# Performance work log

Hardware: AMD Instinct MI355X
Metric: run time of the kernel (lower is better)

Reference implementation:

```python
import jax, jax.numpy as jnp
import numpy as np

RATE_NUM = 8
MAX_RATE = 256
C = 256


def setup_inputs() -> dict:
    key = jax.random.key(0)
    k1, k2, k3, k4 = jax.random.split(key, 4)
    B, H, W = 4, 32, 32
    x = jax.random.normal(k1, (B, MAX_RATE, H, W), dtype=jnp.float32)
    indexes = jax.random.randint(k2, (B * H * W,), 0, RATE_NUM, dtype=jnp.int64)
    # kaiming_normal_(a=sqrt(5)) on (rate_num, max_rate, C): fan_in = C (last dim),
    # gain = sqrt(2/(1+a^2)) = sqrt(1/3), std = gain/sqrt(fan_in)
    std = np.sqrt(1.0 / 3.0) / np.sqrt(C)
    weight = jax.random.normal(k3, (RATE_NUM, MAX_RATE, C), dtype=jnp.float32) * std
    bound = 1.0 / np.sqrt(RATE_NUM)
    bias = jax.random.uniform(k4, (RATE_NUM, C), dtype=jnp.float32, minval=-bound, maxval=bound)
    return {"x": x, "indexes": indexes, "weight": weight, "bias": bias}


def reference(x, indexes, weight, bias):
    B, R, H, W = x.shape  # R == max_rate
    L = H * W
    x_blr = x.reshape(B, R, L).transpose(0, 2, 1)          # (B, L, R)
    w = weight[indexes].reshape(B, L, R, -1)               # (B, L, R, C)
    b = bias[indexes].reshape(B, L, -1)                    # (B, L, C)
    out = jnp.einsum('blr,blrc->blc', x_blr, w) + b        # per-token GEMV
    return out.reshape(B, H, W, -1).transpose(0, 3, 1, 2)  # (B, C, H, W)
```

## Files before the change

kernel.cpp:

```cpp
#include <hip/hip_runtime.h>


#define C_DIM 256
#define KD    256
#define LDP   132

typedef __attribute__((ext_vector_type(8))) short bf16x8;
typedef __attribute__((ext_vector_type(4))) float f32x4;

__device__ inline unsigned pk2(float a, float b) {
    union { float f; unsigned u; } x, y; x.f = a; y.f = b;
    return ((x.u + 0x8000u) >> 16) | ((y.u + 0x8000u) & 0xFFFF0000u);
}

__global__ __launch_bounds__(256) void prep_kernel(
    const float* __restrict__ x, const float* __restrict__ w,
    unsigned* __restrict__ wbd, unsigned* __restrict__ xbd)
{
    const int g = blockIdx.x * 256 + threadIdx.x;
    if (blockIdx.x < 256) {
        const int f  = g * 4;
        const int j  = f >> 15;
        const int ct = (f >> 14) & 1;
        const int kp = (f >> 7) & 127;
        const int cl = f & 124;
        const float4 a = *(const float4*)(w + ((j * 256 + 2 * kp    ) << 8) + ct * 128 + cl);
        const float4 b = *(const float4*)(w + ((j * 256 + 2 * kp + 1) << 8) + ct * 128 + cl);
        uint4 o;
        o.x = pk2(a.x, b.x); o.y = pk2(a.y, b.y);
        o.z = pk2(a.z, b.z); o.w = pk2(a.w, b.w);
        *(uint4*)(wbd + f) = o;
    } else {
        const int g2 = g - 65536;
        const int f  = g2 * 4;
        const int b_ = f >> 17;
        const int lt = (f >> 14) & 7;
        const int kp = (f >> 7) & 127;
        const int ll = f & 124;
        const float4 a = *(const float4*)(x + ((b_ * 256 + 2 * kp    ) << 10) + lt * 128 + ll);
        const float4 c = *(const float4*)(x + ((b_ * 256 + 2 * kp + 1) << 10) + lt * 128 + ll);
        uint4 o;
        o.x = pk2(a.x, c.x); o.y = pk2(a.y, c.y);
        o.z = pk2(a.z, c.z); o.w = pk2(a.w, c.w);
        *(uint4*)(xbd + f) = o;
    }
}

__global__ __launch_bounds__(512, 4) void fused_mfma_kernel(
    const unsigned* __restrict__ wbd,
    const unsigned* __restrict__ xbd,
    const int*      __restrict__ idx,
    const float*    __restrict__ bias,
    float*          __restrict__ out)
{
    const int t    = threadIdx.x;
    const int lane = t & 63;
    const int wav  = t >> 6;
    const int quad = lane >> 4;
    const int li   = lane & 15;

    const int j    = blockIdx.z;
    const int ct   = blockIdx.x;
    const int cb0  = ct * 128;
    const int lg0b = blockIdx.y * 128;
    const int b    = lg0b >> 10;
    const int l0b  = lg0b & 1023;
    const int lt   = (lg0b >> 7) & 7;

    __shared__ unsigned Asl[2][32 * LDP];
    __shared__ unsigned Bsl[2][32 * LDP];

    const unsigned* __restrict__ wsrc = wbd + ((j * 2 + ct) << 14);
    const unsigned* __restrict__ xsrc = xbd + ((b * 8 + lt) << 14);

    const int u0 = t, u1 = 512 + t;
    const int la0 = (u0 >> 5) * LDP + (u0 & 31) * 4;
    const int la1 = (u1 >> 5) * LDP + (u1 & 31) * 4;

    const int wc = wav & 3;
    const int wl = wav >> 2;
    const int c_locb = wc * 32;
    const int l_locb = wl * 64;

    f32x4 acc[2][4];
    #pragma unroll
    for (int mt = 0; mt < 2; ++mt)
        #pragma unroll
        for (int nt = 0; nt < 4; ++nt)
            acc[mt][nt] = (f32x4){0.f, 0.f, 0.f, 0.f};

    uint4 a0 = *(const uint4*)(wsrc + u0 * 4);
    uint4 a1 = *(const uint4*)(wsrc + u1 * 4);
    uint4 b0 = *(const uint4*)(xsrc + u0 * 4);
    uint4 b1 = *(const uint4*)(xsrc + u1 * 4);
    *(uint4*)&Asl[0][la0] = a0;
    *(uint4*)&Asl[0][la1] = a1;
    *(uint4*)&Bsl[0][la0] = b0;
    *(uint4*)&Bsl[0][la1] = b1;
    __syncthreads();

    #pragma unroll
    for (int p = 0; p < 4; ++p) {
        if (p < 3) {
            const int off = (p + 1) * 4096;
            a0 = *(const uint4*)(wsrc + off + u0 * 4);
            a1 = *(const uint4*)(wsrc + off + u1 * 4);
            b0 = *(const uint4*)(xsrc + off + u0 * 4);
            b1 = *(const uint4*)(xsrc + off + u1 * 4);
        }

        const unsigned* __restrict__ Ab = Asl[p & 1];
        const unsigned* __restrict__ Bb = Bsl[p & 1];
        #pragma unroll
        for (int h = 0; h < 2; ++h) {
            const int rbase = h * 16 + quad * 4;
            bf16x8 af[2], bfr[4];
            #pragma unroll
            for (int mt = 0; mt < 2; ++mt) {
                const int cl = c_locb + mt * 16 + li;
                uint4 u;
                u.x = Ab[(rbase + 0) * LDP + cl];
                u.y = Ab[(rbase + 1) * LDP + cl];
                u.z = Ab[(rbase + 2) * LDP + cl];
                u.w = Ab[(rbase + 3) * LDP + cl];
                af[mt] = __builtin_bit_cast(bf16x8, u);
            }
            #pragma unroll
            for (int nt = 0; nt < 4; ++nt) {
                const int ll = l_locb + nt * 16 + li;
                uint4 u;
                u.x = Bb[(rbase + 0) * LDP + ll];
                u.y = Bb[(rbase + 1) * LDP + ll];
                u.z = Bb[(rbase + 2) * LDP + ll];
                u.w = Bb[(rbase + 3) * LDP + ll];
                bfr[nt] = __builtin_bit_cast(bf16x8, u);
            }
            #pragma unroll
            for (int mt = 0; mt < 2; ++mt)
                #pragma unroll
                for (int nt = 0; nt < 4; ++nt)
                    acc[mt][nt] = __builtin_amdgcn_mfma_f32_16x16x32_bf16(
                        af[mt], bfr[nt], acc[mt][nt], 0, 0, 0);
        }

        if (p < 3) {
            const int q = (p + 1) & 1;
            *(uint4*)&Asl[q][la0] = a0;
            *(uint4*)&Asl[q][la1] = a1;
            *(uint4*)&Bsl[q][la0] = b0;
            *(uint4*)&Bsl[q][la1] = b1;
            __syncthreads();
        }
    }

    bool keep[4];
    int  lgv[4];
    #pragma unroll
    for (int nt = 0; nt < 4; ++nt) {
        lgv[nt]  = lg0b + l_locb + nt * 16 + li;
        keep[nt] = (idx[lgv[nt]] == j);
    }
    #pragma unroll
    for (int mt = 0; mt < 2; ++mt) {
        const int cb = cb0 + c_locb + mt * 16 + quad * 4;
        const float4 bb = *(const float4*)(bias + j * C_DIM + cb);
        #pragma unroll
        for (int nt = 0; nt < 4; ++nt) {
            if (!keep[nt]) continue;
            float* __restrict__ op = out + (b << 18) + (cb << 10) + (lgv[nt] & 1023);
            op[0 << 10] = acc[mt][nt][0] + bb.x;
            op[1 << 10] = acc[mt][nt][1] + bb.y;
            op[2 << 10] = acc[mt][nt][2] + bb.z;
            op[3 << 10] = acc[mt][nt][3] + bb.w;
        }
    }
}

extern "C" void kernel_launch(void* const* d_in, const int* in_sizes, int n_in,
                              void* d_out, int out_size, void* d_ws, size_t ws_size,
                              hipStream_t stream)
{
    const float* x      = (const float*)d_in[0];
    const int*   idx    = (const int*)  d_in[1];
    const float* weight = (const float*)d_in[2];
    const float* bias   = (const float*)d_in[3];
    float*       out    = (float*)      d_out;

    unsigned* wbd = (unsigned*)d_ws;
    unsigned* xbd = wbd + (1 << 18);

    prep_kernel<<<768, 256, 0, stream>>>(x, weight, wbd, xbd);

    fused_mfma_kernel<<<dim3(2, 32, 8), 512, 0, stream>>>(wbd, xbd, idx, bias, out);
}
```

Baseline: 72.31 us.

## Pre-pack bf16 operands in MFMA fragment order and stream via global_load_lds

The prep kernel now packs 8 consecutive K values per column into one 16-byte fragment, so the main kernel reads each MFMA operand with a single 16-byte LDS load instead of four scalar loads. Tiles are copied from global memory straight into LDS with global_load_lds, skipping the register round trip, and the K loop is split into 8 smaller stages. The idx load is also hoisted before the main loop. Risks: global_load_lds completion may not be guaranteed by the plain barrier, the LDS layout no longer has padding, and the prep kernel's strided scalar reads are less coalesced.

```diff
diff --git a/kernel.cpp b/kernel.cpp
--- a/kernel.cpp
+++ b/kernel.cpp
@@ -2,8 +2,6 @@
 
 
 #define C_DIM 256
-#define KD    256
-#define LDP   132
 
 typedef __attribute__((ext_vector_type(8))) short bf16x8;
 typedef __attribute__((ext_vector_type(4))) float f32x4;
@@ -13,36 +11,43 @@
     return ((x.u + 0x8000u) >> 16) | ((y.u + 0x8000u) & 0xFFFF0000u);
 }
 
+__device__ inline void gl16(const unsigned* g, unsigned* l) {
+    __builtin_amdgcn_global_load_lds(
+        (const __attribute__((address_space(1))) unsigned*)g,
+        (__attribute__((address_space(3))) unsigned*)l, 16, 0, 0);
+}
+
 __global__ __launch_bounds__(256) void prep_kernel(
-    const float* __restrict__ x, const float* __restrict__ w,
+    const float* __restrict__ x, const float* __restrict__ wt,
     unsigned* __restrict__ wbd, unsigned* __restrict__ xbd)
 {
-    const int g = blockIdx.x * 256 + threadIdx.x;
+    const int tid = threadIdx.x;
     if (blockIdx.x < 256) {
-        const int f  = g * 4;
-        const int j  = f >> 15;
-        const int ct = (f >> 14) & 1;
-        const int kp = (f >> 7) & 127;
-        const int cl = f & 124;
-        const float4 a = *(const float4*)(w + ((j * 256 + 2 * kp    ) << 8) + ct * 128 + cl);
-        const float4 b = *(const float4*)(w + ((j * 256 + 2 * kp + 1) << 8) + ct * 128 + cl);
+        const int g  = blockIdx.x * 256 + tid;
+        const int c  = g & 127;
+        const int gg = (g >> 7) & 31;
+        const int ct = (g >> 12) & 1;
+        const int j  = g >> 13;
+        const float* src = wt + ((j * 256 + gg * 8) << 8) + ct * 128 + c;
         uint4 o;
-        o.x = pk2(a.x, b.x); o.y = pk2(a.y, b.y);
-        o.z = pk2(a.z, b.z); o.w = pk2(a.w, b.w);
-        *(uint4*)(wbd + f) = o;
+        o.x = pk2(src[0 << 8], src[1 << 8]);
+        o.y = pk2(src[2 << 8], src[3 << 8]);
+        o.z = pk2(src[4 << 8], src[5 << 8]);
+        o.w = pk2(src[6 << 8], src[7 << 8]);
+        *(uint4*)(wbd + (size_t)g * 4) = o;
     } else {
-        const int g2 = g - 65536;
-        const int f  = g2 * 4;
-        const int b_ = f >> 17;
-        const int lt = (f >> 14) & 7;
-        const int kp = (f >> 7) & 127;
-        const int ll = f & 124;
-        const float4 a = *(const float4*)(x + ((b_ * 256 + 2 * kp    ) << 10) + lt * 128 + ll);
-        const float4 c = *(const float4*)(x + ((b_ * 256 + 2 * kp + 1) << 10) + lt * 128 + ll);
+        const int h  = (blockIdx.x - 256) * 256 + tid;
+        const int ll = h & 127;
+        const int gg = (h >> 7) & 31;
+        const int lt = (h >> 12) & 7;
+        const int b  = h >> 15;
+        const float* src = x + ((b * 256 + gg * 8) << 10) + lt * 128 + ll;
         uint4 o;
-        o.x = pk2(a.x, c.x); o.y = pk2(a.y, c.y);
-        o.z = pk2(a.z, c.z); o.w = pk2(a.w, c.w);
-        *(uint4*)(xbd + f) = o;
+        o.x = pk2(src[0 << 10], src[1 << 10]);
+        o.y = pk2(src[2 << 10], src[3 << 10]);
+        o.z = pk2(src[4 << 10], src[5 << 10]);
+        o.w = pk2(src[6 << 10], src[7 << 10]);
+        *(uint4*)(xbd + (size_t)h * 4) = o;
     }
 }
 
@@ -64,23 +69,26 @@
     const int cb0  = ct * 128;
     const int lg0b = blockIdx.y * 128;
     const int b    = lg0b >> 10;
-    const int l0b  = lg0b & 1023;
     const int lt   = (lg0b >> 7) & 7;
 
-    __shared__ unsigned Asl[2][32 * LDP];
-    __shared__ unsigned Bsl[2][32 * LDP];
+    __shared__ __align__(16) unsigned Asl[2][2048];
+    __shared__ __align__(16) unsigned Bsl[2][2048];
 
-    const unsigned* __restrict__ wsrc = wbd + ((j * 2 + ct) << 14);
-    const unsigned* __restrict__ xsrc = xbd + ((b * 8 + lt) << 14);
-
-    const int u0 = t, u1 = 512 + t;
-    const int la0 = (u0 >> 5) * LDP + (u0 & 31) * 4;
-    const int la1 = (u1 >> 5) * LDP + (u1 & 31) * 4;
+    const unsigned* __restrict__ wsrc = wbd + ((size_t)(j * 2 + ct) << 14);
+    const unsigned* __restrict__ xsrc = xbd + ((size_t)(b * 8 + lt) << 14);
 
     const int wc = wav & 3;
     const int wl = wav >> 2;
     const int c_locb = wc * 32;
     const int l_locb = wl * 64;
+
+    bool keep[4];
+    int  lgv[4];
+    #pragma unroll
+    for (int nt = 0; nt < 4; ++nt) {
+        lgv[nt]  = lg0b + l_locb + nt * 16 + li;
+        keep[nt] = (idx[lgv[nt]] == j);
+    }
 
     f32x4 acc[2][4];
     #pragma unroll
@@ -89,77 +97,45 @@
         for (int nt = 0; nt < 4; ++nt)
             acc[mt][nt] = (f32x4){0.f, 0.f, 0.f, 0.f};
 
-    uint4 a0 = *(const uint4*)(wsrc + u0 * 4);
-    uint4 a1 = *(const uint4*)(wsrc + u1 * 4);
-    uint4 b0 = *(const uint4*)(xsrc + u0 * 4);
-    uint4 b1 = *(const uint4*)(xsrc + u1 * 4);
-    *(uint4*)&Asl[0][la0] = a0;
-    *(uint4*)&Asl[0][la1] = a1;
-    *(uint4*)&Bsl[0][la0] = b0;
-    *(uint4*)&Bsl[0][la1] = b1;
+    const int t4 = t * 4;
+
+    gl16(wsrc + t4, &Asl[0][t4]);
+    gl16(xsrc + t4, &Bsl[0][t4]);
     __syncthreads();
 
     #pragma unroll
-    for (int p = 0; p < 4; ++p) {
-        if (p < 3) {
-            const int off = (p + 1) * 4096;
-            a0 = *(const uint4*)(wsrc + off + u0 * 4);
-            a1 = *(const uint4*)(wsrc + off + u1 * 4);
-            b0 = *(const uint4*)(xsrc + off + u0 * 4);
-            b1 = *(const uint4*)(xsrc + off + u1 * 4);
+    for (int p = 0; p < 8; ++p) {
+        if (p < 7) {
+            const int off = (p + 1) * 2048;
+            gl16(wsrc + off + t4, &Asl[(p + 1) & 1][t4]);
+            gl16(xsrc + off + t4, &Bsl[(p + 1) & 1][t4]);
         }
 
         const unsigned* __restrict__ Ab = Asl[p & 1];
         const unsigned* __restrict__ Bb = Bsl[p & 1];
+        bf16x8 af[2], bfr[4];
         #pragma unroll
-        for (int h = 0; h < 2; ++h) {
-            const int rbase = h * 16 + quad * 4;
-            bf16x8 af[2], bfr[4];
+        for (int mt = 0; mt < 2; ++mt) {
+            const int cl = c_locb + mt * 16 + li;
+            af[mt] = __builtin_bit_cast(bf16x8,
+                *(const uint4*)&Ab[quad * 512 + cl * 4]);
+        }
+        #pragma unroll
+        for (int nt = 0; nt < 4; ++nt) {
+            const int ll = l_locb + nt * 16 + li;
+            bfr[nt] = __builtin_bit_cast(bf16x8,
+                *(const uint4*)&Bb[quad * 512 + ll * 4]);
+        }
+        #pragma unroll
+        for (int mt = 0; mt < 2; ++mt)
             #pragma unroll
-            for (int mt = 0; mt < 2; ++mt) {
-                const int cl = c_locb + mt * 16 + li;
-                uint4 u;
-                u.x = Ab[(rbase + 0) * LDP + cl];
-                u.y = Ab[(rbase + 1) * LDP + cl];
-                u.z = Ab[(rbase + 2) * LDP + cl];
-                u.w = Ab[(rbase + 3) * LDP + cl];
-                af[mt] = __builtin_bit_cast(bf16x8, u);
-            }
-            #pragma unroll
-            for (int nt = 0; nt < 4; ++nt) {
-                const int ll = l_locb + nt * 16 + li;
-                uint4 u;
-                u.x = Bb[(rbase + 0) * LDP + ll];
-                u.y = Bb[(rbase + 1) * LDP + ll];
-                u.z = Bb[(rbase + 2) * LDP + ll];
-                u.w = Bb[(rbase + 3) * LDP + ll];
-                bfr[nt] = __builtin_bit_cast(bf16x8, u);
-            }
-            #pragma unroll
-            for (int mt = 0; mt < 2; ++mt)
-                #pragma unroll
-                for (int nt = 0; nt < 4; ++nt)
-                    acc[mt][nt] = __builtin_amdgcn_mfma_f32_16x16x32_bf16(
-                        af[mt], bfr[nt], acc[mt][nt], 0, 0, 0);
-        }
+            for (int nt = 0; nt < 4; ++nt)
+                acc[mt][nt] = __builtin_amdgcn_mfma_f32_16x16x32_bf16(
+                    af[mt], bfr[nt], acc[mt][nt], 0, 0, 0);
 
-        if (p < 3) {
-            const int q = (p + 1) & 1;
-            *(uint4*)&Asl[q][la0] = a0;
-            *(uint4*)&Asl[q][la1] = a1;
-            *(uint4*)&Bsl[q][la0] = b0;
-            *(uint4*)&Bsl[q][la1] = b1;
-            __syncthreads();
-        }
+        if (p < 7) __syncthreads();
     }
 
-    bool keep[4];
-    int  lgv[4];
-    #pragma unroll
-    for (int nt = 0; nt < 4; ++nt) {
-        lgv[nt]  = lg0b + l_locb + nt * 16 + li;
-        keep[nt] = (idx[lgv[nt]] == j);
-    }
     #pragma unroll
     for (int mt = 0; mt < 2; ++mt) {
         const int cb = cb0 + c_locb + mt * 16 + quad * 4;
```

New measurement: 71.92 us. About the same (-0.5%).
